# Optimization experiments

Measured on AMD Instinct MI355X. Metric: run time of the kernel, lower is better.

Reference implementation:

```python
import jax, jax.numpy as jnp
import numpy as np

K_CURV = 1.0   # manifold curvature k
KERNEL = 5
STRIDE = 1
PAD = 2


def setup_inputs() -> dict:
    key = jax.random.key(0)
    k1, k2, k3 = jax.random.split(key, 3)
    bsz, L, Cin, Cout = 16, 8192, 64, 64
    # Build points on the Lorentz manifold: time = sqrt(||space||^2 + k)
    space = jax.random.normal(k1, (bsz, L, Cin - 1), dtype=jnp.float32)
    time = jnp.sqrt(jnp.sum(space ** 2, axis=-1, keepdims=True) + K_CURV)
    x = jnp.concatenate([time, space], axis=-1)  # (bs, len, Cin)
    lin_feat = (Cin - 1) * KERNEL + 1            # 316
    W = jax.random.normal(k2, (Cout, lin_feat), dtype=jnp.float32) / np.sqrt(lin_feat).astype(np.float32)
    b = jax.random.normal(k3, (Cout,), dtype=jnp.float32) * 0.01
    return {"x": x, "W": W, "b": b}


def reference(x, W, b):
    bsz, L, C = x.shape
    sqrt_k = jnp.sqrt(jnp.asarray(K_CURV, x.dtype))
    # pad along length, then clamp time component to sqrt(k) (F.pad + clamp_)
    xp = jnp.pad(x, ((0, 0), (PAD, PAD), (0, 0)))
    xp = xp.at[..., 0].set(jnp.maximum(xp[..., 0], sqrt_k))
    L_out = (L + 2 * PAD - KERNEL) // STRIDE + 1
    # unfold(1, K, stride): gather overlapping windows -> (bs, L_out, K, C)
    idx = jnp.arange(L_out)[:, None] * STRIDE + jnp.arange(KERNEL)[None, :]
    patches = xp[:, idx, :]
    patches = jnp.swapaxes(patches, 2, 3)        # (bs, L_out, C, K) as torch unfold
    # Lorentz time rescale over the K time coords of each patch
    p_time = patches[:, :, 0, :]                 # (bs, L_out, K)
    t_resc = jnp.sqrt(jnp.sum(p_time ** 2, axis=-1, keepdims=True)
                      - (KERNEL - 1) * K_CURV)   # (bs, L_out, 1)
    p_space = patches[:, :, 1:, :].reshape(bsz, L_out, -1)  # (bs, L_out, (C-1)*K)
    feats = jnp.concatenate([t_resc, p_space], axis=-1)     # (bs, L_out, lin_feat)
    # LorentzFullyConnected: linear, then recompute time from space norm
    y = jnp.einsum('blf,of->blo', feats, W) + b              # (bs, L_out, Cout)
    y_space = y[..., 1:]
    y_time = jnp.sqrt(jnp.sum(y_space ** 2, axis=-1, keepdims=True) + K_CURV)
    return jnp.concatenate([y_time, y_space], axis=-1)
```

## Files before the change

### kernel.cpp

```cpp
#include <hip/hip_runtime.h>
#include <math.h>


#define BSZ   16
#define LLEN  8192
#define CIN   64
#define COUT  64
#define KW    5
#define LINF  316
#define MTILE 128
#define ROWS  (MTILE + 4)
#define ASTR  72
#define KB    320

typedef __attribute__((ext_vector_type(8))) short  short8;
typedef __attribute__((ext_vector_type(4))) float  float4v;

__device__ inline unsigned short f2bf(float f) {
    unsigned u = __builtin_bit_cast(unsigned int, f);
    u += 0x7FFFu + ((u >> 16) & 1u);
    return (unsigned short)(u >> 16);
}

__global__ __launch_bounds__(256) void prep_W(const float* __restrict__ W,
                                              unsigned short* __restrict__ Wb) {
    int i = blockIdx.x * 256 + threadIdx.x;
    if (i >= COUT * KB) return;
    int n   = i / KB;
    int kk  = i - n * KB;
    int tap = kk >> 6;
    int c   = kk & 63;
    float v = (c == 0) ? 0.f : W[n * LINF + 1 + (c - 1) * KW + tap];
    Wb[i] = f2bf(v);
}

__global__ __launch_bounds__(256) void lorentz_mfma(
    const float* __restrict__ x, const unsigned short* __restrict__ Wb,
    const float* __restrict__ W, const float* __restrict__ bias,
    float* __restrict__ out)
{
    __shared__ unsigned short At[ROWS * ASTR];
    __shared__ float tcol[ROWS];
    __shared__ float trsc[MTILE];

    int tid = threadIdx.x;
    int blk = blockIdx.x;
    int b   = blk >> 6;
    int l0  = (blk & 63) * MTILE;
    const float* xb = x + ((size_t)b * LLEN) * CIN;

    for (int i = tid; i < ROWS * 16; i += 256) {
        int r = i >> 4, ch = i & 15;
        int row = l0 - 2 + r;
        bool inr = (row >= 0) && (row < LLEN);
        int rowc = min(max(row, 0), LLEN - 1);
        float4 v = ((const float4*)(xb + (size_t)rowc * CIN))[ch];
        if (!inr) { v.x = (ch == 0) ? 1.f : 0.f; v.y = 0.f; v.z = 0.f; v.w = 0.f; }
        if (ch == 0) tcol[r] = v.x;
        ushort4 pk;
        pk.x = f2bf(v.x); pk.y = f2bf(v.y); pk.z = f2bf(v.z); pk.w = f2bf(v.w);
        *(ushort4*)&At[r * ASTR + ch * 4] = pk;
    }
    __syncthreads();

    if (tid < MTILE) {
        float s = 0.f;
        #pragma unroll
        for (int k = 0; k < KW; ++k) { float t = tcol[tid + k]; s += t * t; }
        trsc[tid] = sqrtf(s - (float)(KW - 1));
    }
    __syncthreads();

    int lane = tid & 63, wv = tid >> 6;
    int col = lane & 15, quad = lane >> 4;
    int m0 = wv * 32;

    float4v acc[2][4];
    #pragma unroll
    for (int s = 0; s < 2; ++s)
        #pragma unroll
        for (int nt = 0; nt < 4; ++nt)
            acc[s][nt] = (float4v){0.f, 0.f, 0.f, 0.f};

    #pragma unroll
    for (int tap = 0; tap < KW; ++tap) {
        #pragma unroll
        for (int ks = 0; ks < 2; ++ks) {
            short8 bfr[4];
            #pragma unroll
            for (int nt = 0; nt < 4; ++nt) {
                int n = nt * 16 + col;
                bfr[nt] = *(const short8*)(Wb + n * KB + tap * 64 + ks * 32 + quad * 8);
            }
            short8 afr[2];
            #pragma unroll
            for (int s = 0; s < 2; ++s) {
                int row = m0 + s * 16 + col + tap;
                afr[s] = *(const short8*)&At[row * ASTR + ks * 32 + quad * 8];
            }
            #pragma unroll
            for (int s = 0; s < 2; ++s)
                #pragma unroll
                for (int nt = 0; nt < 4; ++nt)
                    acc[s][nt] = __builtin_amdgcn_mfma_f32_16x16x32_bf16(
                        afr[s], bfr[nt], acc[s][nt], 0, 0, 0);
        }
    }

    float bo[4], w0[4];
    #pragma unroll
    for (int nt = 0; nt < 4; ++nt) {
        int o = nt * 16 + col;
        bo[nt] = bias[o];
        w0[nt] = W[o * LINF];
    }
    size_t obase = (size_t)blk * MTILE;
    #pragma unroll
    for (int s = 0; s < 2; ++s) {
        float y[4][4];
        float ssq[4] = {0.f, 0.f, 0.f, 0.f};
        #pragma unroll
        for (int reg = 0; reg < 4; ++reg) {
            float tr = trsc[m0 + s * 16 + quad * 4 + reg];
            #pragma unroll
            for (int nt = 0; nt < 4; ++nt) {
                float v = acc[s][nt][reg] + bo[nt] + tr * w0[nt];
                y[nt][reg] = v;
                bool isc0 = (nt == 0) && (col == 0);
                ssq[reg] += isc0 ? 0.f : v * v;
            }
        }
        #pragma unroll
        for (int reg = 0; reg < 4; ++reg) {
            #pragma unroll
            for (int msk = 1; msk < 16; msk <<= 1)
                ssq[reg] += __shfl_xor(ssq[reg], msk, 64);
            if (col == 0) y[0][reg] = sqrtf(ssq[reg] + 1.f);
        }
        #pragma unroll
        for (int reg = 0; reg < 4; ++reg) {
            size_t pos = obase + m0 + s * 16 + quad * 4 + reg;
            float* orow = out + pos * COUT;
            #pragma unroll
            for (int nt = 0; nt < 4; ++nt)
                orow[nt * 16 + col] = y[nt][reg];
        }
    }
}

extern "C" void kernel_launch(void* const* d_in, const int* in_sizes, int n_in,
                              void* d_out, int out_size, void* d_ws, size_t ws_size,
                              hipStream_t stream) {
    const float* x    = (const float*)d_in[0];
    const float* W    = (const float*)d_in[1];
    const float* bias = (const float*)d_in[2];
    float* out = (float*)d_out;
    unsigned short* Wb = (unsigned short*)d_ws;

    hipLaunchKernelGGL(prep_W, dim3((COUT * KB + 255) / 256), dim3(256), 0, stream,
                       W, Wb);
    hipLaunchKernelGGL(lorentz_mfma, dim3(BSZ * LLEN / MTILE), dim3(256), 0, stream,
                       x, Wb, W, bias, out);
}
```

Before: 112.6 us.

## Halve row tile per block and compute time rescale in registers

Reduces the rows per block from 128 to 64, doubling the grid to 2048 blocks, and gives each wave one 16-row MFMA subtile instead of two. The Lorentz time rescale is now computed per thread from the shared time column, which removes the trsc shared array and one barrier. The load loop is also fully unrolled with a fixed trip count. This adds occupancy and parallelism, at the cost of more halo rows and more W fragment reloads per output row.

```diff
diff --git a/kernel.cpp b/kernel.cpp
--- a/kernel.cpp
+++ b/kernel.cpp
@@ -8,7 +8,7 @@
 #define COUT  64
 #define KW    5
 #define LINF  316
-#define MTILE 128
+#define MTILE 64
 #define ROWS  (MTILE + 4)
 #define ASTR  72
 #define KB    320
@@ -41,69 +41,66 @@
 {
     __shared__ unsigned short At[ROWS * ASTR];
     __shared__ float tcol[ROWS];
-    __shared__ float trsc[MTILE];
 
     int tid = threadIdx.x;
     int blk = blockIdx.x;
-    int b   = blk >> 6;
-    int l0  = (blk & 63) * MTILE;
+    int b   = blk >> 7;
+    int l0  = (blk & 127) * MTILE;
     const float* xb = x + ((size_t)b * LLEN) * CIN;
 
-    for (int i = tid; i < ROWS * 16; i += 256) {
-        int r = i >> 4, ch = i & 15;
-        int row = l0 - 2 + r;
-        bool inr = (row >= 0) && (row < LLEN);
-        int rowc = min(max(row, 0), LLEN - 1);
-        float4 v = ((const float4*)(xb + (size_t)rowc * CIN))[ch];
-        if (!inr) { v.x = (ch == 0) ? 1.f : 0.f; v.y = 0.f; v.z = 0.f; v.w = 0.f; }
-        if (ch == 0) tcol[r] = v.x;
-        ushort4 pk;
-        pk.x = f2bf(v.x); pk.y = f2bf(v.y); pk.z = f2bf(v.z); pk.w = f2bf(v.w);
-        *(ushort4*)&At[r * ASTR + ch * 4] = pk;
-    }
-    __syncthreads();
-
-    if (tid < MTILE) {
-        float s = 0.f;
-        #pragma unroll
-        for (int k = 0; k < KW; ++k) { float t = tcol[tid + k]; s += t * t; }
-        trsc[tid] = sqrtf(s - (float)(KW - 1));
+    #pragma unroll
+    for (int it = 0; it < 5; ++it) {
+        int i = tid + it * 256;
+        if (i < ROWS * 16) {
+            int r = i >> 4, ch = i & 15;
+            int row = l0 - 2 + r;
+            bool inr = (row >= 0) && (row < LLEN);
+            int rowc = min(max(row, 0), LLEN - 1);
+            float4 v = ((const float4*)(xb + (size_t)rowc * CIN))[ch];
+            if (!inr) { v.x = (ch == 0) ? 1.f : 0.f; v.y = 0.f; v.z = 0.f; v.w = 0.f; }
+            if (ch == 0) tcol[r] = v.x;
+            ushort4 pk;
+            pk.x = f2bf(v.x); pk.y = f2bf(v.y); pk.z = f2bf(v.z); pk.w = f2bf(v.w);
+            *(ushort4*)&At[r * ASTR + ch * 4] = pk;
+        }
     }
     __syncthreads();
 
     int lane = tid & 63, wv = tid >> 6;
     int col = lane & 15, quad = lane >> 4;
-    int m0 = wv * 32;
+    int m0 = wv * 16;
 
-    float4v acc[2][4];
+    float tw[8];
+    {
+        const float4* tp = (const float4*)&tcol[m0 + quad * 4];
+        float4 a = tp[0], c = tp[1];
+        tw[0] = a.x; tw[1] = a.y; tw[2] = a.z; tw[3] = a.w;
+        tw[4] = c.x; tw[5] = c.y; tw[6] = c.z; tw[7] = c.w;
+    }
+    float trsc[4];
     #pragma unroll
-    for (int s = 0; s < 2; ++s)
+    for (int reg = 0; reg < 4; ++reg) {
+        float s = 0.f;
         #pragma unroll
-        for (int nt = 0; nt < 4; ++nt)
-            acc[s][nt] = (float4v){0.f, 0.f, 0.f, 0.f};
+        for (int t = 0; t < KW; ++t) { float v = tw[reg + t]; s += v * v; }
+        trsc[reg] = sqrtf(s - (float)(KW - 1));
+    }
+
+    float4v acc[4];
+    #pragma unroll
+    for (int nt = 0; nt < 4; ++nt) acc[nt] = (float4v){0.f, 0.f, 0.f, 0.f};
 
     #pragma unroll
     for (int tap = 0; tap < KW; ++tap) {
         #pragma unroll
         for (int ks = 0; ks < 2; ++ks) {
-            short8 bfr[4];
+            short8 afr = *(const short8*)&At[(m0 + col + tap) * ASTR + ks * 32 + quad * 8];
             #pragma unroll
             for (int nt = 0; nt < 4; ++nt) {
-                int n = nt * 16 + col;
-                bfr[nt] = *(const short8*)(Wb + n * KB + tap * 64 + ks * 32 + quad * 8);
+                short8 bfr = *(const short8*)(Wb + (nt * 16 + col) * KB
+                                              + tap * 64 + ks * 32 + quad * 8);
+                acc[nt] = __builtin_amdgcn_mfma_f32_16x16x32_bf16(afr, bfr, acc[nt], 0, 0, 0);
             }
-            short8 afr[2];
-            #pragma unroll
-            for (int s = 0; s < 2; ++s) {
-                int row = m0 + s * 16 + col + tap;
-                afr[s] = *(const short8*)&At[row * ASTR + ks * 32 + quad * 8];
-            }
-            #pragma unroll
-            for (int s = 0; s < 2; ++s)
-                #pragma unroll
-                for (int nt = 0; nt < 4; ++nt)
-                    acc[s][nt] = __builtin_amdgcn_mfma_f32_16x16x32_bf16(
-                        afr[s], bfr[nt], acc[s][nt], 0, 0, 0);
         }
     }
 
@@ -114,37 +111,32 @@
         bo[nt] = bias[o];
         w0[nt] = W[o * LINF];
     }
-    size_t obase = (size_t)blk * MTILE;
+    float y[4][4];
+    float ssq[4] = {0.f, 0.f, 0.f, 0.f};
     #pragma unroll
-    for (int s = 0; s < 2; ++s) {
-        float y[4][4];
-        float ssq[4] = {0.f, 0.f, 0.f, 0.f};
+    for (int reg = 0; reg < 4; ++reg) {
         #pragma unroll
-        for (int reg = 0; reg < 4; ++reg) {
-            float tr = trsc[m0 + s * 16 + quad * 4 + reg];
-            #pragma unroll
-            for (int nt = 0; nt < 4; ++nt) {
-                float v = acc[s][nt][reg] + bo[nt] + tr * w0[nt];
-                y[nt][reg] = v;
-                bool isc0 = (nt == 0) && (col == 0);
-                ssq[reg] += isc0 ? 0.f : v * v;
-            }
+        for (int nt = 0; nt < 4; ++nt) {
+            float v = acc[nt][reg] + bo[nt] + trsc[reg] * w0[nt];
+            y[nt][reg] = v;
+            bool isc0 = (nt == 0) && (col == 0);
+            ssq[reg] += isc0 ? 0.f : v * v;
         }
+    }
+    #pragma unroll
+    for (int reg = 0; reg < 4; ++reg) {
         #pragma unroll
-        for (int reg = 0; reg < 4; ++reg) {
-            #pragma unroll
-            for (int msk = 1; msk < 16; msk <<= 1)
-                ssq[reg] += __shfl_xor(ssq[reg], msk, 64);
-            if (col == 0) y[0][reg] = sqrtf(ssq[reg] + 1.f);
-        }
+        for (int msk = 1; msk < 16; msk <<= 1)
+            ssq[reg] += __shfl_xor(ssq[reg], msk, 64);
+        if (col == 0) y[0][reg] = sqrtf(ssq[reg] + 1.f);
+    }
+    size_t obase = (size_t)blk * MTILE + m0;
+    #pragma unroll
+    for (int reg = 0; reg < 4; ++reg) {
+        float* orow = out + (obase + quad * 4 + reg) * COUT;
         #pragma unroll
-        for (int reg = 0; reg < 4; ++reg) {
-            size_t pos = obase + m0 + s * 16 + quad * 4 + reg;
-            float* orow = out + pos * COUT;
-            #pragma unroll
-            for (int nt = 0; nt < 4; ++nt)
-                orow[nt * 16 + col] = y[nt][reg];
-        }
+        for (int nt = 0; nt < 4; ++nt)
+            orow[nt * 16 + col] = y[nt][reg];
     }
 }
 
```

After: 123.7 us. +9.9%, slower.
